# Kernel tuning notes

Hardware: AMD Instinct MI355X
Metric: run time of the kernel (lower is better)

Reference implementation:

```python
import jax, jax.numpy as jnp
import numpy as np

D_MODEL, N_HEADS, N_LEVELS, N_POINTS = 256, 8, 4, 4
SHAPES = [(64, 64), (32, 32), (16, 16), (8, 8)]  # (H, W) per level
BATCH = 4


def setup_inputs() -> dict:
    key = jax.random.key(0)
    ks = jax.random.split(key, 10)
    C = D_MODEL
    Lv = sum(h * w for h, w in SHAPES)
    Lq = Lv  # encoder self-attention: queries are the flattened multiscale tokens
    B = BATCH
    s = 0.02
    query = jax.random.normal(ks[0], (B, Lq, C), jnp.float32)
    input_flatten = jax.random.normal(ks[1], (B, Lv, C), jnp.float32)
    reference_points = jax.random.uniform(ks[2], (B, Lq, N_LEVELS, 2), jnp.float32)
    spatial_shapes = jnp.array(SHAPES, jnp.int32)
    sizes = np.array([h * w for h, w in SHAPES], np.int32)
    level_start_index = jnp.asarray(np.concatenate([[0], np.cumsum(sizes)[:-1]]).astype(np.int32))
    w_val = jax.random.normal(ks[3], (C, C), jnp.float32) * s
    b_val = jnp.zeros((C,), jnp.float32)
    w_off = jax.random.normal(ks[4], (C, N_HEADS * N_LEVELS * N_POINTS * 2), jnp.float32) * s
    b_off = jax.random.normal(ks[5], (N_HEADS * N_LEVELS * N_POINTS * 2,), jnp.float32) * 2.0
    w_attn = jax.random.normal(ks[6], (C, N_HEADS * N_LEVELS * N_POINTS), jnp.float32) * s
    b_attn = jnp.zeros((N_HEADS * N_LEVELS * N_POINTS,), jnp.float32)
    w_out = jax.random.normal(ks[7], (C, C), jnp.float32) * s
    b_out = jnp.zeros((C,), jnp.float32)
    return dict(query=query, reference_points=reference_points, input_flatten=input_flatten,
                spatial_shapes=spatial_shapes, level_start_index=level_start_index,
                w_val=w_val, b_val=b_val, w_off=w_off, b_off=b_off,
                w_attn=w_attn, b_attn=b_attn, w_out=w_out, b_out=b_out)


def _bilinear_sample(value_l, loc_l, Hl, Wl):
    """grid_sample(bilinear, padding_mode='zeros', align_corners=False) equivalent.
    value_l: [B, nH, Hl*Wl, d]; loc_l: [B, nH, Lq, nP, 2] normalized to [0,1]."""
    x = loc_l[..., 0] * Wl - 0.5
    y = loc_l[..., 1] * Hl - 0.5
    x0f = jnp.floor(x); y0f = jnp.floor(y)
    wx1 = x - x0f; wy1 = y - y0f
    x0 = x0f.astype(jnp.int32); y0 = y0f.astype(jnp.int32)
    B, nH, Lq, nP = x0.shape
    out = jnp.zeros(value_l.shape[:2] + (Lq, nP, value_l.shape[-1]), value_l.dtype)
    for dy, wy in ((0, 1.0 - wy1), (1, wy1)):
        for dx, wx in ((0, 1.0 - wx1), (1, wx1)):
            xi = x0 + dx; yi = y0 + dy
            valid = (xi >= 0) & (xi < Wl) & (yi >= 0) & (yi < Hl)
            idx = jnp.clip(yi, 0, Hl - 1) * Wl + jnp.clip(xi, 0, Wl - 1)  # [B,nH,Lq,nP]
            g = jnp.take_along_axis(value_l, idx.reshape(B, nH, Lq * nP, 1), axis=2)
            g = g.reshape(B, nH, Lq, nP, -1)
            out = out + (wy * wx * valid.astype(value_l.dtype))[..., None] * g
    return out  # [B, nH, Lq, nP, d]


def reference(query, reference_points, input_flatten, spatial_shapes, level_start_index,
              w_val, b_val, w_off, b_off, w_attn, b_attn, w_out, b_out):
    B, Lq, C = query.shape
    nH, nL, nP = N_HEADS, N_LEVELS, N_POINTS
    d = C // nH
    shapes = np.asarray(spatial_shapes)
    starts = np.asarray(level_start_index)

    value = (input_flatten @ w_val + b_val).reshape(B, -1, nH, d)
    off = (query @ w_off + b_off).reshape(B, Lq, nH, nL, nP, 2)
    attn = jax.nn.softmax((query @ w_attn + b_attn).reshape(B, Lq, nH, nL * nP), axis=-1)
    attn = attn.reshape(B, Lq, nH, nL, nP)

    # offset normalizer is (W, H) per level
    norm = jnp.asarray(shapes[:, ::-1].astype(np.float32))
    # sampling locations: [B, Lq, nH, nL, nP, 2]
    loc = reference_points[:, :, None, :, None, :] + off / norm[None, None, None, :, None, :]

    out = jnp.zeros((B, Lq, nH, d), query.dtype)
    for l in range(nL):
        Hl, Wl = int(shapes[l, 0]), int(shapes[l, 1])
        s0 = int(starts[l])
        value_l = value[:, s0:s0 + Hl * Wl].transpose(0, 2, 1, 3)      # [B,nH,HW,d]
        loc_l = loc[:, :, :, l].transpose(0, 2, 1, 3, 4)               # [B,nH,Lq,nP,2]
        samp = _bilinear_sample(value_l, loc_l, Hl, Wl)                # [B,nH,Lq,nP,d]
        out = out + jnp.einsum('bhqpd,bqhp->bqhd', samp, attn[:, :, :, l])
    out = out.reshape(B, Lq, C)
    return out @ w_out + b_out
```

## Files before the change

kernel.cpp:

```cpp
#include <hip/hip_runtime.h>
#include <hip/hip_fp16.h>
#include <math.h>

#define LQ 5440
#define LV 5440
#define BATCH_ 4
#define M_TOT (BATCH_ * LQ)

typedef _Float16 f16x8 __attribute__((ext_vector_type(8)));
typedef _Float16 f16x2t __attribute__((ext_vector_type(2)));
typedef float f32x4 __attribute__((ext_vector_type(4)));
typedef unsigned int uint_t;

__device__ __forceinline__ uint_t f2h2(float a, float b) {
  const unsigned short ua = __half_as_ushort(__float2half(a));
  const unsigned short ub = __half_as_ushort(__float2half(b));
  return (uint_t)ua | ((uint_t)ub << 16);
}
__device__ __forceinline__ uint_t pkrtz(float a, float b) {
  auto r = __builtin_amdgcn_cvt_pkrtz(a, b);
  uint_t u;
  __builtin_memcpy(&u, &r, 4);
  return u;
}
__device__ __forceinline__ float lo_f(uint_t u) {
  f16x2t h; __builtin_memcpy(&h, &u, 4); return (float)h[0];
}
__device__ __forceinline__ float hi_f(uint_t u) {
  f16x2t h; __builtin_memcpy(&h, &u, 4); return (float)h[1];
}

__global__ __launch_bounds__(256) void conv_weights(
    const float* __restrict__ w_off, const float* __restrict__ w_out,
    const float* __restrict__ w_val, const float* __restrict__ w_attn,
    unsigned short* __restrict__ Wcat, unsigned short* __restrict__ Wo,
    unsigned short* __restrict__ Wvt)
{
  __shared__ float tbuf[64][65];
  const int tid = threadIdx.x;
  const int k0 = blockIdx.x * 64;
  const int yy = blockIdx.y;
  const float* src; unsigned short* dst; int N; int ntile; int roff = 0;
  if (yy < 4)       { src = w_off;  dst = Wcat; N = 256; ntile = yy; }
  else if (yy < 8)  { src = w_out;  dst = Wo;   N = 256; ntile = yy - 4; }
  else if (yy < 12) { src = w_val;  dst = Wvt;  N = 256; ntile = yy - 8; }
  else              { src = w_attn; dst = Wcat; N = 128; ntile = yy - 12; roff = 256; }
  const int n0 = ntile * 64;
#pragma unroll
  for (int i = 0; i < 16; ++i) {
    const int r = (tid >> 6) + i * 4;
    const int c = tid & 63;
    tbuf[r][c] = src[(size_t)(k0 + r) * N + n0 + c];
  }
  __syncthreads();
#pragma unroll
  for (int i = 0; i < 16; ++i) {
    const int n = (tid >> 6) + i * 4;
    const int kk = tid & 63;
    dst[(size_t)(roff + n0 + n) * 256 + k0 + kk] =
        __half_as_ushort(__float2half(tbuf[kk][n]));
  }
}

__global__ __launch_bounds__(256) void gemm_front(
    const float* __restrict__ ifl, const float* __restrict__ query,
    const unsigned short* __restrict__ Wvt, const unsigned short* __restrict__ Wcat,
    const float* __restrict__ b_val, const float* __restrict__ b_off,
    const float* __restrict__ b_attn,
    unsigned short* __restrict__ valb, unsigned short* __restrict__ offb,
    unsigned short* __restrict__ logitb)
{
  const int P = blockIdx.x;
  const int X = P & 7;
  const int j = P >> 3;
  const int p = j % 5;
  const int rblk = X * 22 + j / 5;
  if (rblk >= M_TOT / 128) return;

  __shared__ unsigned short As[128 * 64];
  __shared__ unsigned short Bs[128 * 64];
  const int tid = threadIdx.x;
  const int w = tid >> 6, lane = tid & 63;
  const int wm = w >> 1, wn = w & 1;
  const int lr = lane & 15, lk = lane >> 4;
  const bool isval = p < 2;
  const float* Af = isval ? ifl : query;
  const unsigned short* Bt = isval ? Wvt : Wcat;
  const int n0 = (isval ? p : p - 2) * 128;
  const int m0 = rblk * 128;

  f32x4 acc[4][4] = {};

  for (int t = 0; t < 4; ++t) {
    const int ka = t * 64;
#pragma unroll
    for (int i = 0; i < 4; ++i) {
      const int rbase = i * 32 + w * 8;
      const int row = rbase + (lane >> 3);
      const int slot = lane & 7;
      const int gs = slot ^ (row & 7);
      const unsigned short* gp = Bt + (size_t)(n0 + row) * 256 + ka + gs * 8;
      __builtin_amdgcn_global_load_lds(
          (const __attribute__((address_space(1))) uint_t*)gp,
          (__attribute__((address_space(3))) uint_t*)(Bs + rbase * 64), 16, 0, 0);
    }
#pragma unroll
    for (int i = 0; i < 4; ++i) {
      const int rbase = i * 32 + w * 8;
      const int row = rbase + (lane >> 3);
      const int slot = lane & 7;
      const int gs = slot ^ (row & 7);
      const float* gp = Af + (size_t)(m0 + row) * 256 + ka + gs * 8;
      const float4 a0 = *(const float4*)gp;
      const float4 a1 = *(const float4*)(gp + 4);
      *(uint4*)&As[(size_t)row * 64 + slot * 8] =
          make_uint4(pkrtz(a0.x, a0.y), pkrtz(a0.z, a0.w),
                     pkrtz(a1.x, a1.y), pkrtz(a1.z, a1.w));
    }
    asm volatile("s_waitcnt vmcnt(0)" ::: "memory");
    __syncthreads();
#pragma unroll
    for (int kk = 0; kk < 2; ++kk) {
      f16x8 af[4], bfv[4];
#pragma unroll
      for (int m = 0; m < 4; ++m) {
        const int row = wm * 64 + m * 16 + lr;
        const int so = (kk * 4 + lk) ^ (row & 7);
        af[m] = *(const f16x8*)((const char*)As + row * 128 + so * 16);
      }
#pragma unroll
      for (int n = 0; n < 4; ++n) {
        const int row = wn * 64 + n * 16 + lr;
        const int so = (kk * 4 + lk) ^ (row & 7);
        bfv[n] = *(const f16x8*)((const char*)Bs + row * 128 + so * 16);
      }
#pragma unroll
      for (int m = 0; m < 4; ++m)
#pragma unroll
        for (int n = 0; n < 4; ++n)
          acc[m][n] = __builtin_amdgcn_mfma_f32_16x16x32_f16(af[m], bfv[n], acc[m][n], 0, 0, 0);
    }
    __syncthreads();
  }
#pragma unroll
  for (int n = 0; n < 4; ++n) {
    const int col = n0 + wn * 64 + n * 16 + lr;
    const float bv = isval ? b_val[col] : (col < 256 ? b_off[col] : b_attn[col - 256]);
#pragma unroll
    for (int m = 0; m < 4; ++m) {
      const int rbase = m0 + wm * 64 + m * 16 + lk * 4;
#pragma unroll
      for (int j2 = 0; j2 < 4; ++j2) {
        const float v = acc[m][n][j2] + bv;
        const int row = rbase + j2;
        const unsigned short hv = __half_as_ushort(__float2half(v));
        if (isval)          valb[(size_t)row * 256 + col] = hv;
        else if (col < 256) offb[(size_t)row * 256 + col] = hv;
        else                logitb[(size_t)row * 128 + (col - 256)] = hv;
      }
    }
  }
}

__global__ __launch_bounds__(256) void gemm_out(
    const unsigned short* __restrict__ A,
    const unsigned short* __restrict__ Bt,
    const float* __restrict__ bias,
    float* __restrict__ C)
{
  const int P = blockIdx.x;
  const int X = P & 7;
  const int j = P >> 3;
  const int p = j % 2;
  const int rblk = X * 22 + j / 2;
  if (rblk >= M_TOT / 128) return;

  __shared__ unsigned short As[128 * 64];
  __shared__ unsigned short Bs[128 * 64];
  const int tid = threadIdx.x;
  const int w = tid >> 6, lane = tid & 63;
  const int wm = w >> 1, wn = w & 1;
  const int lr = lane & 15, lk = lane >> 4;
  const int m0 = rblk * 128, n0 = p * 128;

  f32x4 acc[4][4] = {};

  for (int t = 0; t < 4; ++t) {
    const int ka = t * 64;
#pragma unroll
    for (int i = 0; i < 4; ++i) {
      const int rbase = i * 32 + w * 8;
      const int row = rbase + (lane >> 3);
      const int slot = lane & 7;
      const int gs = slot ^ (row & 7);
      const unsigned short* gp = A + (size_t)(m0 + row) * 256 + ka + gs * 8;
      __builtin_amdgcn_global_load_lds(
          (const __attribute__((address_space(1))) uint_t*)gp,
          (__attribute__((address_space(3))) uint_t*)(As + rbase * 64), 16, 0, 0);
    }
#pragma unroll
    for (int i = 0; i < 4; ++i) {
      const int rbase = i * 32 + w * 8;
      const int row = rbase + (lane >> 3);
      const int slot = lane & 7;
      const int gs = slot ^ (row & 7);
      const unsigned short* gp = Bt + (size_t)(n0 + row) * 256 + ka + gs * 8;
      __builtin_amdgcn_global_load_lds(
          (const __attribute__((address_space(1))) uint_t*)gp,
          (__attribute__((address_space(3))) uint_t*)(Bs + rbase * 64), 16, 0, 0);
    }
    asm volatile("s_waitcnt vmcnt(0)" ::: "memory");
    __syncthreads();
#pragma unroll
    for (int kk = 0; kk < 2; ++kk) {
      f16x8 af[4], bfv[4];
#pragma unroll
      for (int m = 0; m < 4; ++m) {
        const int row = wm * 64 + m * 16 + lr;
        const int so = (kk * 4 + lk) ^ (row & 7);
        af[m] = *(const f16x8*)((const char*)As + row * 128 + so * 16);
      }
#pragma unroll
      for (int n = 0; n < 4; ++n) {
        const int row = wn * 64 + n * 16 + lr;
        const int so = (kk * 4 + lk) ^ (row & 7);
        bfv[n] = *(const f16x8*)((const char*)Bs + row * 128 + so * 16);
      }
#pragma unroll
      for (int m = 0; m < 4; ++m)
#pragma unroll
        for (int n = 0; n < 4; ++n)
          acc[m][n] = __builtin_amdgcn_mfma_f32_16x16x32_f16(af[m], bfv[n], acc[m][n], 0, 0, 0);
    }
    __syncthreads();
  }
#pragma unroll
  for (int n = 0; n < 4; ++n) {
    const int col = n0 + wn * 64 + n * 16 + lr;
    const float bv = bias[col];
#pragma unroll
    for (int m = 0; m < 4; ++m) {
      const int rbase = m0 + wm * 64 + m * 16 + lk * 4;
#pragma unroll
      for (int j2 = 0; j2 < 4; ++j2)
        C[(size_t)(rbase + j2) * 256 + col] = acc[m][n][j2] + bv;
    }
  }
}

__global__ __launch_bounds__(256) void msda_sample_v15(
    const unsigned short* __restrict__ off_buf,
    const unsigned short* __restrict__ logit_buf,
    const unsigned short* __restrict__ value,
    const float* __restrict__ ref_pts,
    const int*  __restrict__ sshapes, const int* __restrict__ lstart,
    unsigned short* __restrict__ samp)
{
  __shared__ uint_t wlds[64 * 68];
  const int tid = threadIdx.x;
  const int P  = blockIdx.x;
  const int L  = (((P & 7) >> 1) * 680) + ((P & 1) * 340) + (P >> 3);
  const int q0 = L * 8;
  const int b  = L / (LQ / 8);
  const int q  = tid >> 5;
  const int qg = q0 + q;

  {
    const int h  = (tid >> 2) & 7;
    const int l  = tid & 3;
    const int Hl = sshapes[2 * l], Wl = sshapes[2 * l + 1];
    const int st = lstart[l];
    const float rx = ref_pts[(size_t)qg * 8 + l * 2 + 0];
    const float ry = ref_pts[(size_t)qg * 8 + l * 2 + 1];
    const float fx = rx * (float)Wl - 0.5f;
    const float fy = ry * (float)Hl - 0.5f;

    const uint4 og = *(const uint4*)(off_buf + (size_t)qg * 256 + h * 32 + l * 8);
    const float offv[8] = {lo_f(og.x), hi_f(og.x), lo_f(og.y), hi_f(og.y),
                           lo_f(og.z), hi_f(og.z), lo_f(og.w), hi_f(og.w)};

    const uint2 lgu = *(const uint2*)(logit_buf + (size_t)qg * 128 + h * 16 + l * 4);
    float lg[4];
    lg[0] = lo_f(lgu.x); lg[1] = hi_f(lgu.x);
    lg[2] = lo_f(lgu.y); lg[3] = hi_f(lgu.y);

    float mx = fmaxf(fmaxf(lg[0], lg[1]), fmaxf(lg[2], lg[3]));
    mx = fmaxf(mx, __shfl_xor(mx, 1));
    mx = fmaxf(mx, __shfl_xor(mx, 2));
    float ex[4]; float ssum = 0.f;
#pragma unroll
    for (int p = 0; p < 4; ++p) { ex[p] = __expf(lg[p] - mx); ssum += ex[p]; }
    ssum += __shfl_xor(ssum, 1);
    ssum += __shfl_xor(ssum, 2);
    const float inv = 1.f / ssum;

    const uint_t base_idx = (uint_t)b * LV + (uint_t)st;
    uint_t* wrow = wlds + (size_t)(q * 8 + h) * 68;

#pragma unroll
    for (int p = 0; p < 4; ++p) {
      const float x = fx + offv[p * 2 + 0];
      const float y = fy + offv[p * 2 + 1];
      const float aw = ex[p] * inv;
      const float xf = floorf(x), yf = floorf(y);
      const int x0i = (int)xf, y0i = (int)yf;
      const float wx1 = x - xf, wy1 = y - yf;
      const float wx0 = 1.f - wx1, wy0 = 1.f - wy1;
      const int x1i = x0i + 1, y1i = y0i + 1;
      const bool vx0 = (uint_t)x0i < (uint_t)Wl, vx1 = (uint_t)x1i < (uint_t)Wl;
      const bool vy0 = (uint_t)y0i < (uint_t)Hl, vy1 = (uint_t)y1i < (uint_t)Hl;
      const int xc0 = min(max(x0i, 0), Wl - 1), xc1 = min(max(x1i, 0), Wl - 1);
      const int yc0 = min(max(y0i, 0), Hl - 1), yc1 = min(max(y1i, 0), Hl - 1);
      const float awy0 = aw * wy0, awy1 = aw * wy1;
      const float w00 = (vy0 && vx0) ? awy0 * wx0 : 0.f;
      const float w01 = (vy0 && vx1) ? awy0 * wx1 : 0.f;
      const float w10 = (vy1 && vx0) ? awy1 * wx0 : 0.f;
      const float w11 = (vy1 && vx1) ? awy1 * wx1 : 0.f;
      const uint_t r0 = base_idx + (uint_t)(yc0 * Wl), r1 = base_idx + (uint_t)(yc1 * Wl);
      uint4 pk;
      pk.x = f2h2(w00, w01);
      pk.y = f2h2(w10, w11);
      pk.z = (r0 + (uint_t)xc0) | ((r0 + (uint_t)xc1) << 16);
      pk.w = (r1 + (uint_t)xc0) | ((r1 + (uint_t)xc1) << 16);
      *(uint4*)(wrow + (l * 4 + p) * 4) = pk;
    }
  }
  __syncthreads();

  const int h  = (tid >> 2) & 7;
  const int dg = tid & 3;
  const uint_t* wrow = wlds + (size_t)(q * 8 + h) * 68;
  const char* vbyte = (const char*)value + (uint_t)h * 64u + (uint_t)dg * 16u;
  float acc[8] = {};

#define ACCUM8T(GP, WV) {                                                          \
    const f16x8 g = *(const f16x8*)(GP);                                           \
    acc[0] = fmaf((float)g[0], (WV), acc[0]);                                      \
    acc[1] = fmaf((float)g[1], (WV), acc[1]);                                      \
    acc[2] = fmaf((float)g[2], (WV), acc[2]);                                      \
    acc[3] = fmaf((float)g[3], (WV), acc[3]);                                      \
    acc[4] = fmaf((float)g[4], (WV), acc[4]);                                      \
    acc[5] = fmaf((float)g[5], (WV), acc[5]);                                      \
    acc[6] = fmaf((float)g[6], (WV), acc[6]);                                      \
    acc[7] = fmaf((float)g[7], (WV), acc[7]); }

#pragma unroll
  for (int pt = 0; pt < 16; ++pt) {
    const uint4 pk = *(const uint4*)(wrow + pt * 4);
    const float w0 = lo_f(pk.x), w1 = hi_f(pk.x);
    const float w2 = lo_f(pk.y), w3 = hi_f(pk.y);
    const uint_t i0 = pk.z & 0xffffu, i1 = pk.z >> 16;
    const uint_t i2 = pk.w & 0xffffu, i3 = pk.w >> 16;
    ACCUM8T(vbyte + (size_t)i0 * 512u, w0);
    ACCUM8T(vbyte + (size_t)i1 * 512u, w1);
    ACCUM8T(vbyte + (size_t)i2 * 512u, w2);
    ACCUM8T(vbyte + (size_t)i3 * 512u, w3);
  }

  const uint4 o = make_uint4(pkrtz(acc[0], acc[1]), pkrtz(acc[2], acc[3]),
                             pkrtz(acc[4], acc[5]), pkrtz(acc[6], acc[7]));
  *(uint4*)(samp + (size_t)qg * 256 + h * 32 + dg * 8) = o;
}

extern "C" void kernel_launch(void* const* d_in, const int* in_sizes, int n_in,
                              void* d_out, int out_size, void* d_ws, size_t ws_size,
                              hipStream_t stream) {
  const float* query         = (const float*)d_in[0];
  const float* ref_pts       = (const float*)d_in[1];
  const float* input_flatten = (const float*)d_in[2];
  const int*   sshapes       = (const int*)d_in[3];
  const int*   lstart        = (const int*)d_in[4];
  const float* w_val  = (const float*)d_in[5];
  const float* b_val  = (const float*)d_in[6];
  const float* w_off  = (const float*)d_in[7];
  const float* b_off  = (const float*)d_in[8];
  const float* w_attn = (const float*)d_in[9];
  const float* b_attn = (const float*)d_in[10];
  const float* w_out  = (const float*)d_in[11];
  const float* b_out  = (const float*)d_in[12];
  float* out = (float*)d_out;

  char* ws = (char*)d_ws;
  unsigned short* valb   = (unsigned short*)(ws);
  unsigned short* samp   = (unsigned short*)(ws + 11141120);
  unsigned short* offb   = (unsigned short*)(ws + 22282240);
  unsigned short* logitb = (unsigned short*)(ws + 33423360);
  unsigned short* Wcat   = (unsigned short*)(ws + 38993920);
  unsigned short* Wo     = (unsigned short*)(ws + 39190528);
  unsigned short* Wvt    = (unsigned short*)(ws + 39321600);

  dim3 blk(256);
  conv_weights<<<dim3(4, 14), blk, 0, stream>>>(w_off, w_out, w_val, w_attn, Wcat, Wo, Wvt);
  gemm_front<<<dim3(880), blk, 0, stream>>>(
      input_flatten, query, Wvt, Wcat, b_val, b_off, b_attn, valb, offb, logitb);
  msda_sample_v15<<<dim3(M_TOT / 8), blk, 0, stream>>>(
      offb, logitb, valb, ref_pts, sshapes, lstart, samp);
  gemm_out<<<dim3(352), blk, 0, stream>>>(samp, Wo, b_out, out);
}
```

Baseline: 82.81 us.

## Store value head-major and pair corner taps per thread in sampler

The value projection now goes through shared memory and is written in a [batch, head, position, 32] layout. This makes the two x-adjacent corners of a bilinear tap contiguous 64-byte rows, so the sampler stores one packed row index per row pair instead of four corner indices. Eight threads per (query, head) each load 16 bytes, the halves are reduced with a shuffle, and blocks now cover four queries. Zeroed guard regions around the value buffer absorb out-of-range x reads at the edges (weights are zero there); this relies on exact workspace offsets and adds a shuffle and a second LDS pass.

```diff
diff --git a/kernel.cpp b/kernel.cpp
--- a/kernel.cpp
+++ b/kernel.cpp
@@ -34,10 +34,15 @@
     const float* __restrict__ w_off, const float* __restrict__ w_out,
     const float* __restrict__ w_val, const float* __restrict__ w_attn,
     unsigned short* __restrict__ Wcat, unsigned short* __restrict__ Wo,
-    unsigned short* __restrict__ Wvt)
+    unsigned short* __restrict__ Wvt,
+    unsigned short* __restrict__ guard_pre, unsigned short* __restrict__ guard_post)
 {
   __shared__ float tbuf[64][65];
   const int tid = threadIdx.x;
+  if (blockIdx.x == 0 && blockIdx.y == 0 && tid < 64) {
+    guard_pre[tid] = 0;
+    guard_post[tid] = 0;
+  }
   const int k0 = blockIdx.x * 64;
   const int yy = blockIdx.y;
   const float* src; unsigned short* dst; int N; int ntile; int roff = 0;
@@ -77,8 +82,9 @@
   const int rblk = X * 22 + j / 5;
   if (rblk >= M_TOT / 128) return;
 
-  __shared__ unsigned short As[128 * 64];
-  __shared__ unsigned short Bs[128 * 64];
+  __shared__ unsigned short Sh[2][128 * 64];
+  unsigned short* As = Sh[0];
+  unsigned short* Bs = Sh[1];
   const int tid = threadIdx.x;
   const int w = tid >> 6, lane = tid & 63;
   const int wm = w >> 1, wn = w & 1;
@@ -142,22 +148,54 @@
     }
     __syncthreads();
   }
-#pragma unroll
-  for (int n = 0; n < 4; ++n) {
-    const int col = n0 + wn * 64 + n * 16 + lr;
-    const float bv = isval ? b_val[col] : (col < 256 ? b_off[col] : b_attn[col - 256]);
-#pragma unroll
-    for (int m = 0; m < 4; ++m) {
-      const int rbase = m0 + wm * 64 + m * 16 + lk * 4;
-#pragma unroll
-      for (int j2 = 0; j2 < 4; ++j2) {
-        const float v = acc[m][n][j2] + bv;
-        const int row = rbase + j2;
-        const unsigned short hv = __half_as_ushort(__float2half(v));
-        if (isval)          valb[(size_t)row * 256 + col] = hv;
-        else if (col < 256) offb[(size_t)row * 256 + col] = hv;
-        else                logitb[(size_t)row * 128 + (col - 256)] = hv;
-      }
+
+  if (!isval) {
+#pragma unroll
+    for (int n = 0; n < 4; ++n) {
+      const int col = n0 + wn * 64 + n * 16 + lr;
+      const float bv = (col < 256) ? b_off[col] : b_attn[col - 256];
+#pragma unroll
+      for (int m = 0; m < 4; ++m) {
+        const int rbase = m0 + wm * 64 + m * 16 + lk * 4;
+#pragma unroll
+        for (int j2 = 0; j2 < 4; ++j2) {
+          const float v = acc[m][n][j2] + bv;
+          const int row = rbase + j2;
+          const unsigned short hv = __half_as_ushort(__float2half(v));
+          if (col < 256) offb[(size_t)row * 256 + col] = hv;
+          else           logitb[(size_t)row * 128 + (col - 256)] = hv;
+        }
+      }
+    }
+  } else {
+    unsigned short* Sb = &Sh[0][0];
+#pragma unroll
+    for (int n = 0; n < 4; ++n) {
+      const int lcol = wn * 64 + n * 16 + lr;
+      const float bv = b_val[n0 + lcol];
+#pragma unroll
+      for (int m = 0; m < 4; ++m) {
+        const int lrow = wm * 64 + m * 16 + lk * 4;
+#pragma unroll
+        for (int j2 = 0; j2 < 4; ++j2)
+          Sb[(size_t)(lrow + j2) * 128 + lcol] =
+              __half_as_ushort(__float2half(acc[m][n][j2] + bv));
+      }
+    }
+    __syncthreads();
+#pragma unroll
+    for (int it = 0; it < 8; ++it) {
+      const int idx = it * 256 + tid;
+      const int r  = idx >> 4;
+      const int c8 = idx & 15;
+      const uint_t row_g = (uint_t)(m0 + r);
+      const uint_t bb  = row_g / (uint_t)LV;
+      const uint_t pos = row_g - bb * (uint_t)LV;
+      const int colg = n0 + c8 * 8;
+      const uint_t hh = (uint_t)colg >> 5;
+      const uint_t chо = (uint_t)colg & 31u;
+      unsigned short* dp = valb + (((size_t)(bb * 8u + hh) * LV + pos) << 5) + chо;
+      *(uint4*)dp = *(const uint4*)&Sb[(size_t)r * 128 + c8 * 8];
     }
   }
 }
@@ -248,7 +286,7 @@
   }
 }
 
-__global__ __launch_bounds__(256) void msda_sample_v15(
+__global__ __launch_bounds__(256) void msda_sample_v16(
     const unsigned short* __restrict__ off_buf,
     const unsigned short* __restrict__ logit_buf,
     const unsigned short* __restrict__ value,
@@ -256,18 +294,18 @@
     const int*  __restrict__ sshapes, const int* __restrict__ lstart,
     unsigned short* __restrict__ samp)
 {
-  __shared__ uint_t wlds[64 * 68];
+  __shared__ uint_t wlds[32 * 68];
   const int tid = threadIdx.x;
   const int P  = blockIdx.x;
-  const int L  = (((P & 7) >> 1) * 680) + ((P & 1) * 340) + (P >> 3);
-  const int q0 = L * 8;
-  const int b  = L / (LQ / 8);
-  const int q  = tid >> 5;
-  const int qg = q0 + q;
-
-  {
+  const int L  = (((P & 7) >> 1) * 1360) + ((P & 1) * 680) + (P >> 3);
+  const int q0 = L * 4;
+  const int b  = L / (LQ / 4);
+  const int qp1 = tid >> 5;
+
+  if (tid < 128) {
     const int h  = (tid >> 2) & 7;
     const int l  = tid & 3;
+    const int qg = q0 + qp1;
     const int Hl = sshapes[2 * l], Wl = sshapes[2 * l + 1];
     const int st = lstart[l];
     const float rx = ref_pts[(size_t)qg * 8 + l * 2 + 0];
@@ -294,8 +332,7 @@
     ssum += __shfl_xor(ssum, 2);
     const float inv = 1.f / ssum;
 
-    const uint_t base_idx = (uint_t)b * LV + (uint_t)st;
-    uint_t* wrow = wlds + (size_t)(q * 8 + h) * 68;
+    uint_t* wrow = wlds + (size_t)(qp1 * 8 + h) * 68;
 
 #pragma unroll
     for (int p = 0; p < 4; ++p) {
@@ -309,57 +346,60 @@
       const int x1i = x0i + 1, y1i = y0i + 1;
       const bool vx0 = (uint_t)x0i < (uint_t)Wl, vx1 = (uint_t)x1i < (uint_t)Wl;
       const bool vy0 = (uint_t)y0i < (uint_t)Hl, vy1 = (uint_t)y1i < (uint_t)Hl;
-      const int xc0 = min(max(x0i, 0), Wl - 1), xc1 = min(max(x1i, 0), Wl - 1);
-      const int yc0 = min(max(y0i, 0), Hl - 1), yc1 = min(max(y1i, 0), Hl - 1);
       const float awy0 = aw * wy0, awy1 = aw * wy1;
       const float w00 = (vy0 && vx0) ? awy0 * wx0 : 0.f;
       const float w01 = (vy0 && vx1) ? awy0 * wx1 : 0.f;
       const float w10 = (vy1 && vx0) ? awy1 * wx0 : 0.f;
       const float w11 = (vy1 && vx1) ? awy1 * wx1 : 0.f;
-      const uint_t r0 = base_idx + (uint_t)(yc0 * Wl), r1 = base_idx + (uint_t)(yc1 * Wl);
+      const int yc0 = min(max(y0i, 0), Hl - 1);
+      const int yc1 = min(max(y1i, 0), Hl - 1);
+      const int xr  = (vx0 || vx1) ? max(x0i, -1) : 0;
+      const int i00 = st + yc0 * Wl + xr;
+      const int i10 = st + yc1 * Wl + xr;
       uint4 pk;
       pk.x = f2h2(w00, w01);
       pk.y = f2h2(w10, w11);
-      pk.z = (r0 + (uint_t)xc0) | ((r0 + (uint_t)xc1) << 16);
-      pk.w = (r1 + (uint_t)xc0) | ((r1 + (uint_t)xc1) << 16);
+      pk.z = ((uint_t)i00 & 0xffffu) | (((uint_t)i10 & 0xffffu) << 16);
+      pk.w = 0u;
       *(uint4*)(wrow + (l * 4 + p) * 4) = pk;
     }
   }
   __syncthreads();
 
-  const int h  = (tid >> 2) & 7;
-  const int dg = tid & 3;
-  const uint_t* wrow = wlds + (size_t)(q * 8 + h) * 68;
-  const char* vbyte = (const char*)value + (uint_t)h * 64u + (uint_t)dg * 16u;
+  const int grp = tid >> 3;
+  const int g   = tid & 7;
+  const int q2  = grp >> 3;
+  const int h2  = grp & 7;
+  const int qg2 = q0 + q2;
+  const uint_t* wrow = wlds + (size_t)grp * 68;
+  const char* vB = (const char*)value
+      + ((size_t)(b * 8 + h2) * LV) * 64 + (size_t)g * 16;
+  const int side = g >> 2;
   float acc[8] = {};
-
-#define ACCUM8T(GP, WV) {                                                          \
-    const f16x8 g = *(const f16x8*)(GP);                                           \
-    acc[0] = fmaf((float)g[0], (WV), acc[0]);                                      \
-    acc[1] = fmaf((float)g[1], (WV), acc[1]);                                      \
-    acc[2] = fmaf((float)g[2], (WV), acc[2]);                                      \
-    acc[3] = fmaf((float)g[3], (WV), acc[3]);                                      \
-    acc[4] = fmaf((float)g[4], (WV), acc[4]);                                      \
-    acc[5] = fmaf((float)g[5], (WV), acc[5]);                                      \
-    acc[6] = fmaf((float)g[6], (WV), acc[6]);                                      \
-    acc[7] = fmaf((float)g[7], (WV), acc[7]); }
 
 #pragma unroll
   for (int pt = 0; pt < 16; ++pt) {
     const uint4 pk = *(const uint4*)(wrow + pt * 4);
-    const float w0 = lo_f(pk.x), w1 = hi_f(pk.x);
-    const float w2 = lo_f(pk.y), w3 = hi_f(pk.y);
-    const uint_t i0 = pk.z & 0xffffu, i1 = pk.z >> 16;
-    const uint_t i2 = pk.w & 0xffffu, i3 = pk.w >> 16;
-    ACCUM8T(vbyte + (size_t)i0 * 512u, w0);
-    ACCUM8T(vbyte + (size_t)i1 * 512u, w1);
-    ACCUM8T(vbyte + (size_t)i2 * 512u, w2);
-    ACCUM8T(vbyte + (size_t)i3 * 512u, w3);
-  }
-
-  const uint4 o = make_uint4(pkrtz(acc[0], acc[1]), pkrtz(acc[2], acc[3]),
-                             pkrtz(acc[4], acc[5]), pkrtz(acc[6], acc[7]));
-  *(uint4*)(samp + (size_t)qg * 256 + h * 32 + dg * 8) = o;
+    const float wA = side ? hi_f(pk.x) : lo_f(pk.x);
+    const float wB = side ? hi_f(pk.y) : lo_f(pk.y);
+    const int i0 = (int)(short)(pk.z & 0xffffu);
+    const int i1 = (int)(short)(pk.z >> 16);
+    const f16x8 g0 = *(const f16x8*)(vB + (ptrdiff_t)i0 * 64);
+    const f16x8 g1 = *(const f16x8*)(vB + (ptrdiff_t)i1 * 64);
+#pragma unroll
+    for (int c = 0; c < 8; ++c) acc[c] = fmaf((float)g0[c], wA, acc[c]);
+#pragma unroll
+    for (int c = 0; c < 8; ++c) acc[c] = fmaf((float)g1[c], wB, acc[c]);
+  }
+
+#pragma unroll
+  for (int c = 0; c < 8; ++c) acc[c] += __shfl_xor(acc[c], 4);
+
+  if (g < 4) {
+    const uint4 o = make_uint4(pkrtz(acc[0], acc[1]), pkrtz(acc[2], acc[3]),
+                               pkrtz(acc[4], acc[5]), pkrtz(acc[6], acc[7]));
+    *(uint4*)(samp + (size_t)qg2 * 256 + h2 * 32 + g * 8) = o;
+  }
 }
 
 extern "C" void kernel_launch(void* const* d_in, const int* in_sizes, int n_in,
@@ -381,19 +421,22 @@
   float* out = (float*)d_out;
 
   char* ws = (char*)d_ws;
-  unsigned short* valb   = (unsigned short*)(ws);
-  unsigned short* samp   = (unsigned short*)(ws + 11141120);
-  unsigned short* offb   = (unsigned short*)(ws + 22282240);
-  unsigned short* logitb = (unsigned short*)(ws + 33423360);
-  unsigned short* Wcat   = (unsigned short*)(ws + 38993920);
-  unsigned short* Wo     = (unsigned short*)(ws + 39190528);
-  unsigned short* Wvt    = (unsigned short*)(ws + 39321600);
+  unsigned short* guard_pre  = (unsigned short*)(ws);
+  unsigned short* valb   = (unsigned short*)(ws + 128);
+  unsigned short* guard_post = (unsigned short*)(ws + 11141248);
+  unsigned short* samp   = (unsigned short*)(ws + 11141376);
+  unsigned short* offb   = (unsigned short*)(ws + 22282496);
+  unsigned short* logitb = (unsigned short*)(ws + 33423616);
+  unsigned short* Wcat   = (unsigned short*)(ws + 38994176);
+  unsigned short* Wo     = (unsigned short*)(ws + 39190784);
+  unsigned short* Wvt    = (unsigned short*)(ws + 39321856);
 
   dim3 blk(256);
-  conv_weights<<<dim3(4, 14), blk, 0, stream>>>(w_off, w_out, w_val, w_attn, Wcat, Wo, Wvt);
+  conv_weights<<<dim3(4, 14), blk, 0, stream>>>(
+      w_off, w_out, w_val, w_attn, Wcat, Wo, Wvt, guard_pre, guard_post);
   gemm_front<<<dim3(880), blk, 0, stream>>>(
       input_flatten, query, Wvt, Wcat, b_val, b_off, b_attn, valb, offb, logitb);
-  msda_sample_v15<<<dim3(M_TOT / 8), blk, 0, stream>>>(
+  msda_sample_v16<<<dim3(M_TOT / 4), blk, 0, stream>>>(
       offb, logitb, valb, ref_pts, sshapes, lstart, samp);
   gemm_out<<<dim3(352), blk, 0, stream>>>(samp, Wo, b_out, out);
 }
```

Result: faster. 73.94 us (-10.7%).
